# Kernel optimization log

Measured on AMD Instinct MI355X. Metric: run time of the kernel, lower is better.

The kernel has to match this reference:

```python
import jax, jax.numpy as jnp
import numpy as np

K = 3
PAD = 1
EPS = 1e-5


def _conv2d(x, w, b):
    y = jax.lax.conv_general_dilated(x, w, window_strides=(1, 1), padding='SAME',
                                     dimension_numbers=('NCHW', 'OIHW', 'NCHW'))
    return y + b[None, :, None, None]


def _bn(x, g, beta, m, v):
    inv = jax.lax.rsqrt(v + EPS)
    return (x - m[None, :, None, None]) * (g * inv)[None, :, None, None] + beta[None, :, None, None]


def _deform_conv2d(x, offset, w, b):
    # torchvision deform_conv2d (v1, no mask), stride=1, pad=1, 3x3 kernel.
    B, Cin, H, W = x.shape
    Cout = w.shape[0]
    # offset: [B, 2*K*K, H, W] -> (dy, dx) per kernel tap
    off = offset.reshape(B, K * K, 2, H, W)
    dy, dx = off[:, :, 0], off[:, :, 1]                     # [B, K2, H, W]
    ii, jj = jnp.meshgrid(jnp.arange(K), jnp.arange(K), indexing='ij')
    ki = (ii.reshape(-1) - PAD).astype(x.dtype)             # [K2]
    kj = (jj.reshape(-1) - PAD).astype(x.dtype)
    py = jnp.arange(H, dtype=x.dtype)[None, None, :, None] + ki[None, :, None, None] + dy
    px = jnp.arange(W, dtype=x.dtype)[None, None, None, :] + kj[None, :, None, None] + dx
    y0 = jnp.floor(py)
    x0 = jnp.floor(px)
    wy = py - y0
    wx = px - x0
    flat = x.reshape(B, Cin, H * W)

    def gather(yc, xc):
        valid = ((yc >= 0) & (yc < H) & (xc >= 0) & (xc < W)).astype(x.dtype)
        yi = jnp.clip(yc, 0, H - 1).astype(jnp.int32)
        xi = jnp.clip(xc, 0, W - 1).astype(jnp.int32)
        idx = (yi * W + xi).reshape(B, -1)                  # [B, K2*H*W]
        g = jax.vmap(lambda f, i: f[:, i])(flat, idx)       # [B, Cin, K2*H*W]
        return g.reshape(B, Cin, K * K, H, W) * valid[:, None]

    v = (gather(y0,     x0    ) * ((1 - wy) * (1 - wx))[:, None]
         + gather(y0,     x0 + 1) * ((1 - wy) * wx)[:, None]
         + gather(y0 + 1, x0    ) * (wy * (1 - wx))[:, None]
         + gather(y0 + 1, x0 + 1) * (wy * wx)[:, None])     # [B, Cin, K2, H, W]
    out = jnp.einsum('bckhw,ock->bohw', v, w.reshape(Cout, Cin, K * K))
    return out + b[None, :, None, None]


def setup_inputs() -> dict:
    key = jax.random.key(0)
    ks = jax.random.split(key, 12)
    d = {}
    d['x'] = jax.random.normal(ks[0], (32, 3, 64, 64), jnp.float32)
    d['offset1_w'] = jax.random.normal(ks[1], (18, 3, 3, 3), jnp.float32) * 0.05
    d['offset1_b'] = jnp.zeros((18,), jnp.float32)
    d['conv1_w'] = jax.random.normal(ks[2], (64, 3, 3, 3), jnp.float32) * 0.1
    d['conv1_b'] = jnp.zeros((64,), jnp.float32)
    d['bn1_gamma'] = jnp.ones((64,), jnp.float32)
    d['bn1_beta'] = jnp.zeros((64,), jnp.float32)
    d['bn1_mean'] = jnp.zeros((64,), jnp.float32)
    d['bn1_var'] = jax.random.uniform(ks[3], (64,), jnp.float32, 0.5, 1.5)
    d['offset2_w'] = jax.random.normal(ks[4], (18, 64, 3, 3), jnp.float32) * 0.02
    d['offset2_b'] = jnp.zeros((18,), jnp.float32)
    d['conv2_w'] = jax.random.normal(ks[5], (128, 64, 3, 3), jnp.float32) * 0.05
    d['conv2_b'] = jnp.zeros((128,), jnp.float32)
    d['bn2_gamma'] = jnp.ones((128,), jnp.float32)
    d['bn2_beta'] = jnp.zeros((128,), jnp.float32)
    d['bn2_mean'] = jnp.zeros((128,), jnp.float32)
    d['bn2_var'] = jax.random.uniform(ks[6], (128,), jnp.float32, 0.5, 1.5)
    d['fc1_w'] = jax.random.normal(ks[7], (256, 128), jnp.float32) * 0.08
    d['fc1_b'] = jnp.zeros((256,), jnp.float32)
    d['fc2_w'] = jax.random.normal(ks[8], (200, 256), jnp.float32) * 0.06
    d['fc2_b'] = jnp.zeros((200,), jnp.float32)
    return d


def reference(x, offset1_w, offset1_b, conv1_w, conv1_b, bn1_gamma, bn1_beta, bn1_mean, bn1_var,
              offset2_w, offset2_b, conv2_w, conv2_b, bn2_gamma, bn2_beta, bn2_mean, bn2_var,
              fc1_w, fc1_b, fc2_w, fc2_b):
    # Eval-mode forward (dropout layers are identity / deterministic).
    off1 = _conv2d(x, offset1_w, offset1_b)
    h = _deform_conv2d(x, off1, conv1_w, conv1_b)
    h = jax.nn.relu(_bn(h, bn1_gamma, bn1_beta, bn1_mean, bn1_var))
    off2 = _conv2d(h, offset2_w, offset2_b)
    h = _deform_conv2d(h, off2, conv2_w, conv2_b)
    h = jax.nn.relu(_bn(h, bn2_gamma, bn2_beta, bn2_mean, bn2_var))
    h = h.mean(axis=(2, 3))                                 # global avg pool -> [B, 128]
    h = jax.nn.relu(h @ fc1_w.T + fc1_b)
    return h @ fc2_w.T + fc2_b
```

## Files before the change

### kernel.cpp

```cpp
#include <hip/hip_runtime.h>

#define EPS 1e-5f

#define W1OT 0
#define W1B  1024
#define W2T  4096
#define W2OB 40960
#define SC1  59392
#define SH1  59456
#define SC2  59520
#define SH2  59648
#define POOL 59776
#define XP   65536
#define H1B  589824
#define W1B_U   2048
#define W2T_U   8192
#define W2OB_U  81920
#define H1B_U   1179648

typedef __attribute__((ext_vector_type(8))) short bhalf8;
typedef __attribute__((ext_vector_type(8))) unsigned short u16x8;
typedef __attribute__((ext_vector_type(4))) float f32x4;

#define BPAD 72
#define OPAD 584
#define APAD 40

struct Tap { int i00, i01, i10, i11; float w00, w01, w10, w11; };

__device__ __forceinline__ Tap make_tap(float py, float px) {
    float y0f = floorf(py), x0f = floorf(px);
    float wy = py - y0f, wx = px - x0f;
    bool by0 = (y0f >= 0.f)  && (y0f < 64.f);
    bool by1 = (y0f >= -1.f) && (y0f < 63.f);
    bool bx0 = (x0f >= 0.f)  && (x0f < 64.f);
    bool bx1 = (x0f >= -1.f) && (x0f < 63.f);
    int y0 = min(max((int)y0f, 0), 63);
    int y1 = min(max((int)y0f + 1, 0), 63);
    int x0 = min(max((int)x0f, 0), 63);
    int x1 = min(max((int)x0f + 1, 0), 63);
    Tap tp;
    tp.i00 = y0 * 64 + x0; tp.i01 = y0 * 64 + x1;
    tp.i10 = y1 * 64 + x0; tp.i11 = y1 * 64 + x1;
    tp.w00 = (by0 && bx0) ? (1.f - wy) * (1.f - wx) : 0.f;
    tp.w01 = (by0 && bx1) ? (1.f - wy) * wx         : 0.f;
    tp.w10 = (by1 && bx0) ? wy * (1.f - wx)         : 0.f;
    tp.w11 = (by1 && bx1) ? wy * wx                 : 0.f;
    return tp;
}

__device__ __forceinline__ ushort f2bf(float f) {
    union { float f; uint u; } a; a.f = f;
    uint u = a.u;
    return (ushort)((u + 0x7fffu + ((u >> 16) & 1u)) >> 16);
}
__device__ __forceinline__ float bf2f(ushort u) {
    union { uint u; float f; } a; a.u = ((uint)u) << 16;
    return a.f;
}

__global__ __launch_bounds__(256) void k_prep(
    const float* __restrict__ x,
    const float* __restrict__ o1w, const float* __restrict__ c1w,
    const float* __restrict__ o2w, const float* __restrict__ c2w,
    const float* __restrict__ c1b, const float* __restrict__ g1,
    const float* __restrict__ be1, const float* __restrict__ m1,
    const float* __restrict__ v1,
    const float* __restrict__ c2b, const float* __restrict__ g2,
    const float* __restrict__ be2, const float* __restrict__ m2,
    const float* __restrict__ v2,
    float* __restrict__ ws) {
    int tid = blockIdx.x * 256 + threadIdx.x;
    ushort* wsu = (ushort*)ws;
    if (tid < 648) {
        int co = tid % 18, tc = tid / 18, c = tc & 3, t = tc >> 2;
        ws[W1OT + tid] = (c < 3) ? o1w[(co * 3 + c) * 9 + t] : 0.f;
    } else if (tid < 2696) {
        int i = tid - 648;
        int n = i >> 5, k = i & 31;
        float v = 0.f;
        if (k < 27) { int c = k % 3, t = k / 3; v = c1w[(n * 3 + c) * 9 + t]; }
        wsu[W1B_U + i] = f2bf(v);
    } else if (tid < 76424) {
        int i = tid - 2696;
        int c = i & 63, n = (i >> 6) & 127, t = i >> 13;
        wsu[W2T_U + i] = f2bf(c2w[(n * 64 + c) * 9 + t]);
    } else if (tid < 94856) {
        int i = tid - 76424;
        int n = i / 576, k = i - n * 576;
        int c = k & 63, t = k >> 6;
        float v = (n < 18) ? o2w[(n * 64 + c) * 9 + t] : 0.f;
        wsu[W2OB_U + i] = f2bf(v);
    } else if (tid < 94920) {
        int i = tid - 94856;
        float s = g1[i] * rsqrtf(v1[i] + EPS);
        ws[SC1 + i] = s;
        ws[SH1 + i] = (c1b[i] - m1[i]) * s + be1[i];
    } else if (tid < 95048) {
        int i = tid - 94920;
        float s = g2[i] * rsqrtf(v2[i] + EPS);
        ws[SC2 + i] = s;
        ws[SH2 + i] = (c2b[i] - m2[i]) * s + be2[i];
    } else if (tid < 99144) {
        ws[POOL + tid - 95048] = 0.f;
    } else if (tid < 230216) {
        int i = tid - 99144;
        int b = i >> 12, hw = i & 4095;
        const float* xpp = x + (size_t)b * 3 * 4096 + hw;
        f32x4 o;
        o[0] = xpp[0]; o[1] = xpp[4096]; o[2] = xpp[8192]; o[3] = 0.f;
        *(f32x4*)(ws + XP + (size_t)i * 4) = o;
    }
}

__global__ __launch_bounds__(256, 4) void k_def1(
    const float* __restrict__ o1b, float* __restrict__ ws) {
    __shared__ ushort Alds[256 * APAD];
    __shared__ ushort Blds[64 * APAD];
    __shared__ float wo[648];
    __shared__ float scl[128];
    int tid = threadIdx.x;
    for (int i = tid; i < 648; i += 256) wo[i] = ws[W1OT + i];
    if (tid < 128) scl[tid] = ws[SC1 + tid];
    {
        const ushort* src = (const ushort*)ws + W1B_U;
        if (tid < 128) {
            int n = tid >> 1, half = (tid & 1) * 16;
            *(uint4*)(Blds + n * APAD + half)     = *(const uint4*)(src + n * 32 + half);
            *(uint4*)(Blds + n * APAD + half + 8) = *(const uint4*)(src + n * 32 + half + 8);
        }
    }
    int g = blockIdx.x;
    int b = (g & 7) * 4 + ((g >> 3) & 3);
    int row0 = (g >> 5) * 4;
    int h = row0 + (tid >> 6), w = tid & 63;
    const float* xp = ws + XP + (size_t)b * 16384;

    float off[18];
#pragma unroll
    for (int i = 0; i < 18; ++i) off[i] = o1b[i];
    __syncthreads();
#pragma unroll
    for (int t = 0; t < 9; ++t) {
        int yy = h + t / 3 - 1, xx = w + t % 3 - 1;
        f32x4 pv = (f32x4)0.f;
        if (yy >= 0 && yy < 64 && xx >= 0 && xx < 64)
            pv = *(const f32x4*)(xp + (yy * 64 + xx) * 4);
#pragma unroll
        for (int c = 0; c < 3; ++c) {
            const float* wp = wo + (t * 4 + c) * 18;
#pragma unroll
            for (int co = 0; co < 18; ++co) off[co] += pv[c] * wp[co];
        }
    }
    ushort ob[32];
#pragma unroll
    for (int i = 0; i < 32; ++i) ob[i] = 0;
#pragma unroll
    for (int t = 0; t < 9; ++t) {
        Tap tp = make_tap((float)(h + t / 3 - 1) + off[2 * t],
                          (float)(w + t % 3 - 1) + off[2 * t + 1]);
        f32x4 c00 = *(const f32x4*)(xp + tp.i00 * 4);
        f32x4 c01 = *(const f32x4*)(xp + tp.i01 * 4);
        f32x4 c10 = *(const f32x4*)(xp + tp.i10 * 4);
        f32x4 c11 = *(const f32x4*)(xp + tp.i11 * 4);
        f32x4 vt = tp.w00 * c00 + tp.w01 * c01 + tp.w10 * c10 + tp.w11 * c11;
        ob[t * 3 + 0] = f2bf(vt[0]);
        ob[t * 3 + 1] = f2bf(vt[1]);
        ob[t * 3 + 2] = f2bf(vt[2]);
    }
    {
        ushort* ar = Alds + tid * APAD;
#pragma unroll
        for (int i = 0; i < 4; ++i)
            *(uint4*)(ar + i * 8) = *(const uint4*)(ob + i * 8);
    }
    __syncthreads();

    int lane = tid & 63, wv = tid >> 6;
    int r = lane & 15, q = lane >> 4;
    bhalf8 bf[4];
#pragma unroll
    for (int nt = 0; nt < 4; ++nt)
        bf[nt] = *(const bhalf8*)(Blds + (nt * 16 + r) * APAD + q * 8);
    f32x4 acc[4][4];
#pragma unroll
    for (int mt = 0; mt < 4; ++mt) {
        bhalf8 af = *(const bhalf8*)(Alds + (wv * 64 + mt * 16 + r) * APAD + q * 8);
#pragma unroll
        for (int nt = 0; nt < 4; ++nt)
            acc[mt][nt] = __builtin_amdgcn_mfma_f32_16x16x32_bf16(af, bf[nt], (f32x4)0.f, 0, 0, 0);
    }
    ushort* hb = (ushort*)ws + H1B_U + (size_t)(b * 4096 + row0 * 64) * 64;
#pragma unroll
    for (int nt = 0; nt < 4; ++nt) {
        int col = nt * 16 + r;
        float s0 = scl[col], s1 = scl[64 + col];
#pragma unroll
        for (int mt = 0; mt < 4; ++mt) {
            int pxl = wv * 64 + mt * 16 + q * 4;
#pragma unroll
            for (int rr = 0; rr < 4; ++rr)
                hb[(size_t)(pxl + rr) * 64 + col] =
                    f2bf(fmaxf(acc[mt][nt][rr] * s0 + s1, 0.f));
        }
    }
}

__global__ __launch_bounds__(256, 4) void k_def2(
    const float* __restrict__ o2b, float* __restrict__ ws) {
    __shared__ ushort smem[32 * OPAD];
    float* offL = (float*)smem;
    ushort* Bdef = smem + 2304;
    int g = blockIdx.x;
    int b = (g & 7) * 4 + ((g >> 3) & 3);
    int row = g >> 5;
    int tid = threadIdx.x, lane = tid & 63, wv = tid >> 6;
    int r = lane & 15, q = lane >> 4;
    int px = wv * 16 + r;
    const ushort* hb = (const ushort*)ws + H1B_U + (size_t)b * 262144;
    const ushort* wB = (const ushort*)ws + W2T_U;
    const ushort* bt = (const ushort*)ws + W2OB_U;

    for (int i = tid; i < 2304; i += 256) {
        int n = i / 72, kk = (i - n * 72) * 8;
        *(uint4*)(smem + n * OPAD + kk) = *(const uint4*)(bt + n * 576 + kk);
    }
    __syncthreads();

    f32x4 acc2[2];
    acc2[0] = (f32x4)0.f; acc2[1] = (f32x4)0.f;
#pragma unroll
    for (int t = 0; t < 9; ++t) {
        int yy = row + t / 3 - 1;
        int xx = px + t % 3 - 1;
        bool val = (yy >= 0 && yy < 64 && xx >= 0 && xx < 64);
        int yyc = min(max(yy, 0), 63), xxc = min(max(xx, 0), 63);
        const ushort* ap = hb + (size_t)(yyc * 64 + xxc) * 64 + q * 8;
#pragma unroll
        for (int ks = 0; ks < 2; ++ks) {
            bhalf8 af = val ? *(const bhalf8*)(ap + ks * 32) : (bhalf8)(short)0;
            int kk = t * 64 + ks * 32 + q * 8;
#pragma unroll
            for (int nt = 0; nt < 2; ++nt) {
                bhalf8 bf = *(const bhalf8*)(smem + (nt * 16 + r) * OPAD + kk);
                acc2[nt] = __builtin_amdgcn_mfma_f32_16x16x32_bf16(af, bf, acc2[nt], 0, 0, 0);
            }
        }
    }
    __syncthreads();
#pragma unroll
    for (int nt = 0; nt < 2; ++nt) {
        int n = nt * 16 + r;
        if (n < 18) {
            float bias = o2b[n];
#pragma unroll
            for (int rr = 0; rr < 4; ++rr)
                offL[(wv * 16 + q * 4 + rr) * 18 + n] = acc2[nt][rr] + bias;
        }
    }
    __syncthreads();

    f32x4 acc[8];
#pragma unroll
    for (int j = 0; j < 8; ++j) acc[j] = (f32x4)0.f;
    int bn = tid >> 1, bc = (tid & 1) * 32;

    for (int t = 0; t < 9; ++t) {
        float oy = offL[px * 18 + 2 * t];
        float ox = offL[px * 18 + 2 * t + 1];
        Tap tp = make_tap((float)(row + t / 3 - 1) + oy,
                          (float)(px + t % 3 - 1) + ox);
        if (t) __syncthreads();
        {
            const uint4* s4 = (const uint4*)(wB + (t * 128 + bn) * 64 + bc);
            uint4 p0 = s4[0], p1 = s4[1], p2 = s4[2], p3 = s4[3];
            ushort* dst = Bdef + bn * BPAD + bc;
            *(uint4*)(dst)      = p0;
            *(uint4*)(dst + 8)  = p1;
            *(uint4*)(dst + 16) = p2;
            *(uint4*)(dst + 24) = p3;
        }
        __syncthreads();
#pragma unroll
        for (int ks = 0; ks < 2; ++ks) {
            int ko = ks * 32 + q * 8;
            bhalf8 bf[8];
#pragma unroll
            for (int nt = 0; nt < 8; ++nt)
                bf[nt] = *(const bhalf8*)(Bdef + (nt * 16 + r) * BPAD + ko);
            u16x8 g00 = *(const u16x8*)(hb + (size_t)tp.i00 * 64 + ko);
            u16x8 g01 = *(const u16x8*)(hb + (size_t)tp.i01 * 64 + ko);
            u16x8 g10 = *(const u16x8*)(hb + (size_t)tp.i10 * 64 + ko);
            u16x8 g11 = *(const u16x8*)(hb + (size_t)tp.i11 * 64 + ko);
            f32x4 lo = (f32x4)0.f, hi = (f32x4)0.f;
#pragma unroll
            for (int j = 0; j < 4; ++j) {
                lo[j] = tp.w00 * bf2f(g00[j]) + tp.w01 * bf2f(g01[j])
                      + tp.w10 * bf2f(g10[j]) + tp.w11 * bf2f(g11[j]);
                hi[j] = tp.w00 * bf2f(g00[j + 4]) + tp.w01 * bf2f(g01[j + 4])
                      + tp.w10 * bf2f(g10[j + 4]) + tp.w11 * bf2f(g11[j + 4]);
            }
            bhalf8 af;
#pragma unroll
            for (int j = 0; j < 4; ++j) {
                af[j]     = (short)f2bf(lo[j]);
                af[j + 4] = (short)f2bf(hi[j]);
            }
#pragma unroll
            for (int nt = 0; nt < 8; ++nt)
                acc[nt] = __builtin_amdgcn_mfma_f32_16x16x32_bf16(af, bf[nt], acc[nt], 0, 0, 0);
        }
    }
    const float* sc = ws + SC2;
    const float* sh = ws + SH2;
    float* pool = ws + POOL;
#pragma unroll
    for (int nt = 0; nt < 8; ++nt) {
        int col = nt * 16 + r;
        float s0 = sc[col], s1 = sh[col];
        float s = 0.f;
#pragma unroll
        for (int rr = 0; rr < 4; ++rr)
            s += fmaxf(acc[nt][rr] * s0 + s1, 0.f);
        s += __shfl_xor(s, 16);
        s += __shfl_xor(s, 32);
        if (lane < 16) atomicAdd(&pool[b * 128 + col], s);
    }
}

__global__ __launch_bounds__(256) void k_fc(
    const float* __restrict__ w1, const float* __restrict__ b1,
    const float* __restrict__ w2, const float* __restrict__ b2,
    const float* __restrict__ ws, float* __restrict__ out) {
    int b = blockIdx.x, o = threadIdx.x;
    __shared__ float pl[128];
    __shared__ float hl[256];
    if (o < 128) pl[o] = ws[POOL + b * 128 + o] * (1.f / 4096.f);
    __syncthreads();
    float s = b1[o];
    const float* wp = w1 + o * 128;
#pragma unroll 8
    for (int c = 0; c < 128; ++c) s += pl[c] * wp[c];
    hl[o] = fmaxf(s, 0.f);
    __syncthreads();
    if (o < 200) {
        float s2 = b2[o];
        const float* wp2 = w2 + o * 256;
#pragma unroll 8
        for (int c = 0; c < 256; ++c) s2 += hl[c] * wp2[c];
        out[b * 200 + o] = s2;
    }
}

extern "C" void kernel_launch(void* const* d_in, const int* in_sizes, int n_in,
                              void* d_out, int out_size, void* d_ws, size_t ws_size,
                              hipStream_t stream) {
    const float* x   = (const float*)d_in[0];
    const float* o1w = (const float*)d_in[1];
    const float* o1b = (const float*)d_in[2];
    const float* c1w = (const float*)d_in[3];
    const float* c1b = (const float*)d_in[4];
    const float* g1  = (const float*)d_in[5];
    const float* be1 = (const float*)d_in[6];
    const float* m1  = (const float*)d_in[7];
    const float* v1  = (const float*)d_in[8];
    const float* o2w = (const float*)d_in[9];
    const float* o2b = (const float*)d_in[10];
    const float* c2w = (const float*)d_in[11];
    const float* c2b = (const float*)d_in[12];
    const float* g2  = (const float*)d_in[13];
    const float* be2 = (const float*)d_in[14];
    const float* m2  = (const float*)d_in[15];
    const float* v2  = (const float*)d_in[16];
    const float* f1w = (const float*)d_in[17];
    const float* f1b = (const float*)d_in[18];
    const float* f2w = (const float*)d_in[19];
    const float* f2b = (const float*)d_in[20];
    float* ws  = (float*)d_ws;
    float* out = (float*)d_out;

    k_prep<<<900, 256, 0, stream>>>(x, o1w, c1w, o2w, c2w,
                                    c1b, g1, be1, m1, v1,
                                    c2b, g2, be2, m2, v2, ws);
    k_def1<<<512, 256, 0, stream>>>(o1b, ws);
    k_def2<<<2048, 256, 0, stream>>>(o2b, ws);
    k_fc<<<32, 256, 0, stream>>>(f1w, f1b, f2w, f2b, ws, out);
}
```

Measured before the change: 288.7 us.

## Double-buffer deform-conv weights via async global-to-LDS loads with XOR swizzle

In k_def2 the per-tap weight slice is now copied with global_load_lds straight into one of two swizzled LDS buffers. The next tap's slice is prefetched while the current tap computes, which removes one of the two barriers per tap. The offset-conv B operand is read directly from global memory instead of being staged in LDS. The bilinear gather now unpacks bf16 pairs with shift and mask on 32-bit words. This depends on the async LDS writes being waited on before the barrier and adds extra global traffic for the offset weights.

```diff
diff --git a/kernel.cpp b/kernel.cpp
--- a/kernel.cpp
+++ b/kernel.cpp
@@ -22,8 +22,6 @@
 typedef __attribute__((ext_vector_type(8))) unsigned short u16x8;
 typedef __attribute__((ext_vector_type(4))) float f32x4;
 
-#define BPAD 72
-#define OPAD 584
 #define APAD 40
 
 struct Tap { int i00, i01, i10, i11; float w00, w01, w10, w11; };
@@ -57,6 +55,31 @@
 __device__ __forceinline__ float bf2f(ushort u) {
     union { uint u; float f; } a; a.u = ((uint)u) << 16;
     return a.f;
+}
+
+__device__ __forceinline__ f32x4 evenf(uint4 u) {
+    union { uint u; float f; } a;
+    f32x4 r;
+    a.u = u.x << 16; r[0] = a.f;
+    a.u = u.y << 16; r[1] = a.f;
+    a.u = u.z << 16; r[2] = a.f;
+    a.u = u.w << 16; r[3] = a.f;
+    return r;
+}
+__device__ __forceinline__ f32x4 oddf(uint4 u) {
+    union { uint u; float f; } a;
+    f32x4 r;
+    a.u = u.x & 0xffff0000u; r[0] = a.f;
+    a.u = u.y & 0xffff0000u; r[1] = a.f;
+    a.u = u.z & 0xffff0000u; r[2] = a.f;
+    a.u = u.w & 0xffff0000u; r[3] = a.f;
+    return r;
+}
+
+__device__ __forceinline__ void gl_lds16(const void* g, void* l) {
+    __builtin_amdgcn_global_load_lds(
+        (const __attribute__((address_space(1))) unsigned int*)g,
+        (__attribute__((address_space(3))) unsigned int*)l, 16, 0, 0);
 }
 
 __global__ __launch_bounds__(256) void k_prep(
@@ -209,9 +232,8 @@
 
 __global__ __launch_bounds__(256, 4) void k_def2(
     const float* __restrict__ o2b, float* __restrict__ ws) {
-    __shared__ ushort smem[32 * OPAD];
-    float* offL = (float*)smem;
-    ushort* Bdef = smem + 2304;
+    __shared__ ushort Bd[2][8192];
+    __shared__ float offL[64 * 18];
     int g = blockIdx.x;
     int b = (g & 7) * 4 + ((g >> 3) & 3);
     int row = g >> 5;
@@ -222,11 +244,15 @@
     const ushort* wB = (const ushort*)ws + W2T_U;
     const ushort* bt = (const ushort*)ws + W2OB_U;
 
-    for (int i = tid; i < 2304; i += 256) {
-        int n = i / 72, kk = (i - n * 72) * 8;
-        *(uint4*)(smem + n * OPAD + kk) = *(const uint4*)(bt + n * 576 + kk);
-    }
-    __syncthreads();
+    {
+        char* ldst = (char*)&Bd[0][0];
+#pragma unroll
+        for (int i = 0; i < 4; ++i) {
+            int lin = wv * 4096 + i * 1024 + lane * 16;
+            int src = lin ^ (((lin >> 7) & 7) << 4);
+            gl_lds16((const char*)wB + src, ldst + wv * 4096 + i * 1024);
+        }
+    }
 
     f32x4 acc2[2];
     acc2[0] = (f32x4)0.f; acc2[1] = (f32x4)0.f;
@@ -243,12 +269,11 @@
             int kk = t * 64 + ks * 32 + q * 8;
 #pragma unroll
             for (int nt = 0; nt < 2; ++nt) {
-                bhalf8 bf = *(const bhalf8*)(smem + (nt * 16 + r) * OPAD + kk);
+                bhalf8 bf = *(const bhalf8*)(bt + (nt * 16 + r) * 576 + kk);
                 acc2[nt] = __builtin_amdgcn_mfma_f32_16x16x32_bf16(af, bf, acc2[nt], 0, 0, 0);
             }
         }
     }
-    __syncthreads();
 #pragma unroll
     for (int nt = 0; nt < 2; ++nt) {
         int n = nt * 16 + r;
@@ -264,53 +289,49 @@
     f32x4 acc[8];
 #pragma unroll
     for (int j = 0; j < 8; ++j) acc[j] = (f32x4)0.f;
-    int bn = tid >> 1, bc = (tid & 1) * 32;
 
     for (int t = 0; t < 9; ++t) {
+        if (t < 8) {
+            const char* wsrc = (const char*)wB + (t + 1) * 16384;
+            char* ldst = (char*)&Bd[(t + 1) & 1][0];
+#pragma unroll
+            for (int i = 0; i < 4; ++i) {
+                int lin = wv * 4096 + i * 1024 + lane * 16;
+                int src = lin ^ (((lin >> 7) & 7) << 4);
+                gl_lds16(wsrc + src, ldst + wv * 4096 + i * 1024);
+            }
+        }
         float oy = offL[px * 18 + 2 * t];
         float ox = offL[px * 18 + 2 * t + 1];
         Tap tp = make_tap((float)(row + t / 3 - 1) + oy,
                           (float)(px + t % 3 - 1) + ox);
-        if (t) __syncthreads();
-        {
-            const uint4* s4 = (const uint4*)(wB + (t * 128 + bn) * 64 + bc);
-            uint4 p0 = s4[0], p1 = s4[1], p2 = s4[2], p3 = s4[3];
-            ushort* dst = Bdef + bn * BPAD + bc;
-            *(uint4*)(dst)      = p0;
-            *(uint4*)(dst + 8)  = p1;
-            *(uint4*)(dst + 16) = p2;
-            *(uint4*)(dst + 24) = p3;
-        }
-        __syncthreads();
+        const ushort* Bq = Bd[t & 1];
 #pragma unroll
         for (int ks = 0; ks < 2; ++ks) {
             int ko = ks * 32 + q * 8;
+            uint4 u00 = *(const uint4*)(hb + (size_t)tp.i00 * 64 + ko);
+            uint4 u01 = *(const uint4*)(hb + (size_t)tp.i01 * 64 + ko);
+            uint4 u10 = *(const uint4*)(hb + (size_t)tp.i10 * 64 + ko);
+            uint4 u11 = *(const uint4*)(hb + (size_t)tp.i11 * 64 + ko);
+            f32x4 ve = tp.w00 * evenf(u00) + tp.w01 * evenf(u01)
+                     + tp.w10 * evenf(u10) + tp.w11 * evenf(u11);
+            f32x4 vo = tp.w00 * oddf(u00) + tp.w01 * oddf(u01)
+                     + tp.w10 * oddf(u10) + tp.w11 * oddf(u11);
+            union { uint u[4]; bhalf8 h; } A;
+#pragma unroll
+            for (int j = 0; j < 4; ++j)
+                A.u[j] = (uint)f2bf(ve[j]) | ((uint)f2bf(vo[j]) << 16);
             bhalf8 bf[8];
 #pragma unroll
+            for (int nt = 0; nt < 8; ++nt) {
+                int us = ((nt * 16 + r) * 64 + ko) ^ ((r & 7) << 3);
+                bf[nt] = *(const bhalf8*)(Bq + us);
+            }
+#pragma unroll
             for (int nt = 0; nt < 8; ++nt)
-                bf[nt] = *(const bhalf8*)(Bdef + (nt * 16 + r) * BPAD + ko);
-            u16x8 g00 = *(const u16x8*)(hb + (size_t)tp.i00 * 64 + ko);
-            u16x8 g01 = *(const u16x8*)(hb + (size_t)tp.i01 * 64 + ko);
-            u16x8 g10 = *(const u16x8*)(hb + (size_t)tp.i10 * 64 + ko);
-            u16x8 g11 = *(const u16x8*)(hb + (size_t)tp.i11 * 64 + ko);
-            f32x4 lo = (f32x4)0.f, hi = (f32x4)0.f;
-#pragma unroll
-            for (int j = 0; j < 4; ++j) {
-                lo[j] = tp.w00 * bf2f(g00[j]) + tp.w01 * bf2f(g01[j])
-                      + tp.w10 * bf2f(g10[j]) + tp.w11 * bf2f(g11[j]);
-                hi[j] = tp.w00 * bf2f(g00[j + 4]) + tp.w01 * bf2f(g01[j + 4])
-                      + tp.w10 * bf2f(g10[j + 4]) + tp.w11 * bf2f(g11[j + 4]);
-            }
-            bhalf8 af;
-#pragma unroll
-            for (int j = 0; j < 4; ++j) {
-                af[j]     = (short)f2bf(lo[j]);
-                af[j + 4] = (short)f2bf(hi[j]);
-            }
-#pragma unroll
-            for (int nt = 0; nt < 8; ++nt)
-                acc[nt] = __builtin_amdgcn_mfma_f32_16x16x32_bf16(af, bf[nt], acc[nt], 0, 0, 0);
-        }
+                acc[nt] = __builtin_amdgcn_mfma_f32_16x16x32_bf16(A.h, bf[nt], acc[nt], 0, 0, 0);
+        }
+        if (t < 8) __syncthreads();
     }
     const float* sc = ws + SC2;
     const float* sh = ws + SH2;
```

Result: slower. 308.5 us (+6.9%).
